# Kernel tuning notes

Measured on AMD Instinct MI355X. Metric: run time of the kernel, lower is better.

The kernel has to match this reference:

```python
import jax, jax.numpy as jnp
import numpy as np

IOU_TH = 0.5      # iou_threshold
SCORE_TH = 0.5    # confidence_threshold (passed as score_threshold to tf NMS)
MAX_DET = 512     # max_detections


def setup_inputs() -> dict:
    key = jax.random.key(0)
    k1, k2, k3 = jax.random.split(key, 3)
    B, N, C = 8, 2048, 80
    # tf.image.non_max_suppression interprets box columns as corners
    # (y1, x1, y2, x2); generate valid corner boxes in [0, 1].
    mins = jax.random.uniform(k1, (B, N, 2), dtype=jnp.float32)
    sizes = jax.random.uniform(k2, (B, N, 2), dtype=jnp.float32) * 0.2 + 0.01
    box_prediction = jnp.concatenate([mins, mins + sizes], axis=-1)  # [B,N,4]
    class_prediction = jax.random.normal(k3, (B, N, C), dtype=jnp.float32) * 2.0
    return {"box_prediction": box_prediction, "class_prediction": class_prediction}


def _nms_single(boxes, cls_pred, conf):
    """Greedy NMS for one image. boxes [N,4], cls_pred [N,C], conf [N].
    Matches tf.image.non_max_suppression semantics (corner-coordinate IoU,
    score threshold, greedy suppression in descending score order),
    then gathers boxes/cls/conf at the kept indices, padded to MAX_DET."""
    N = boxes.shape[0]
    order = jnp.argsort(-conf)                 # descending scores
    b = boxes[order]                            # [N,4]
    c = cls_pred[order]                         # [N,C]
    s = conf[order]                             # [N]

    bb = jax.lax.stop_gradient(b)               # IoU/indices are non-diff
    y1, x1, y2, x2 = bb[:, 0], bb[:, 1], bb[:, 2], bb[:, 3]
    area = (y2 - y1) * (x2 - x1)                # [N]
    ih = jnp.clip(jnp.minimum(y2[:, None], y2[None, :]) -
                  jnp.maximum(y1[:, None], y1[None, :]), 0.0)
    iw = jnp.clip(jnp.minimum(x2[:, None], x2[None, :]) -
                  jnp.maximum(x1[:, None], x1[None, :]), 0.0)
    inter = ih * iw                             # [N,N]
    union = area[:, None] + area[None, :] - inter
    iou = inter / jnp.maximum(union, 1e-9)      # [N,N]

    valid = s > SCORE_TH                        # score_threshold filter
    idxs = jnp.arange(N)

    def step(keep, xs):
        row, i = xs
        # if box i survives, suppress all later boxes overlapping > IOU_TH
        sup = (row > IOU_TH) & (idxs > i) & keep[i]
        return keep & ~sup, None

    keep, _ = jax.lax.scan(step, valid, (iou, idxs))

    # select kept boxes (already sorted by score) padded to MAX_DET
    masked = jnp.where(keep, s, -1.0)
    top_s, top_idx = jax.lax.top_k(jax.lax.stop_gradient(masked), MAX_DET)
    vm = top_s > SCORE_TH                       # validity of each output slot
    out_box = b[top_idx] * vm[:, None].astype(b.dtype)
    out_cls = c[top_idx] * vm[:, None].astype(c.dtype)
    out_conf = jnp.where(vm, s[top_idx], 0.0)
    return out_box, out_cls, out_conf


def reference(box_prediction, class_prediction):
    # from_logits=True branch of the layer
    class_confidence = jnp.max(jax.nn.sigmoid(class_prediction), axis=-1)  # [B,N]
    cls_prob = jax.nn.softmax(class_prediction, axis=-1)                   # [B,N,C]
    nms_box, nms_cls, nms_conf = jax.vmap(_nms_single)(
        box_prediction, cls_prob, class_confidence)
    return nms_box, nms_cls, nms_conf
```

## Files before the change

kernel.cpp:

```cpp
#include <hip/hip_runtime.h>
#include <stdint.h>

#define BB 8
#define NN 2048
#define NC 80
#define MAXDET 512
#define WPR 32


#define ORD_HALF 0xBF000000u

__global__ void k_conf(const float* __restrict__ cls, uint64_t* __restrict__ keys) {
    int gid = blockIdx.x * blockDim.x + threadIdx.x;
    const float4* p = (const float4*)(cls + (size_t)gid * NC);
    float m = -3.0e38f;
#pragma unroll
    for (int i = 0; i < NC / 4; ++i) {
        float4 v = p[i];
        m = fmaxf(m, fmaxf(fmaxf(v.x, v.y), fmaxf(v.z, v.w)));
    }
    float e  = expf(-m);
    float cf = 1.0f / (1.0f + e);
    uint32_t u = __float_as_uint(cf);
    u = (u & 0x80000000u) ? ~u : (u | 0x80000000u);
    int n = gid & (NN - 1);
    keys[gid] = ((uint64_t)u << 32) | (uint32_t)(NN - 1 - n);
}

#define RCHUNK 128
__global__ __launch_bounds__(512) void k_rank(const uint64_t* __restrict__ keys_in,
                                              uint64_t* __restrict__ keys_out,
                                              const float* __restrict__ boxes,
                                              float* __restrict__ sboxes) {
    __shared__ uint64_t sk[NN];
    __shared__ uint16_t part[4][RCHUNK];
    int b = blockIdx.y, t = threadIdx.x;
    const uint64_t* kin = keys_in + (size_t)b * NN;
#pragma unroll
    for (int j = 0; j < NN / 512; ++j)
        sk[t + j * 512] = kin[t + j * 512];
    __syncthreads();
    int sub = t >> 7;
    int el  = t & (RCHUNK - 1);
    int e   = blockIdx.x * RCHUNK + el;
    uint64_t mykey = sk[e];
    int base = sub * (NN / 4);
    int r = 0;
    for (int mm = 0; mm < NN / 4; ++mm)
        r += (sk[base + mm] > mykey) ? 1 : 0;
    part[sub][el] = (uint16_t)r;
    __syncthreads();
    if (t < RCHUNK) {
        int rank = part[0][t] + part[1][t] + part[2][t] + part[3][t];
        keys_out[(size_t)b * NN + rank] = mykey;
        int orig = (NN - 1) - (int)(mykey & 0xFFFFFFFFull);
        ((float4*)sboxes)[(size_t)b * NN + rank] =
            ((const float4*)boxes)[(size_t)b * NN + orig];
    }
}

__global__ void k_sup(const float* __restrict__ sboxes, uint64_t* __restrict__ sup) {
#pragma clang fp contract(off)
    __shared__ float cy1[256], cx1[256], cy2[256], cx2[256], car[256];
    __shared__ float ry1[64], rx1[64], ry2[64], rx2[64], rar[64];
    int rt = blockIdx.x, ct = blockIdx.y, b = blockIdx.z;
    int t = threadIdx.x;
    int col0 = ct << 8, row0 = rt << 6;
    {
        float4 bx = ((const float4*)sboxes)[(size_t)b * NN + col0 + t];
        cy1[t] = bx.x; cx1[t] = bx.y; cy2[t] = bx.z; cx2[t] = bx.w;
        car[t] = (bx.z - bx.x) * (bx.w - bx.y);
        if (t < 64) {
            float4 rb = ((const float4*)sboxes)[(size_t)b * NN + row0 + t];
            ry1[t] = rb.x; rx1[t] = rb.y; ry2[t] = rb.z; rx2[t] = rb.w;
            rar[t] = (rb.z - rb.x) * (rb.w - rb.y);
        }
    }
    __syncthreads();
    int lr = t & 63, lg = t >> 6;
    int r = row0 + lr;
    int gw = (ct << 2) + lg;
    int cbase = gw << 6;
    uint64_t w = 0;
    if (cbase + 63 > r) {
        float y1 = ry1[lr], x1 = rx1[lr], y2 = ry2[lr], x2 = rx2[lr], ar = rar[lr];
        int lcb = lg << 6;
        for (int c = 0; c < 64; ++c) {
            int lc = lcb + c;
            float ih = fmaxf(fminf(y2, cy2[lc]) - fmaxf(y1, cy1[lc]), 0.0f);
            float iw = fmaxf(fminf(x2, cx2[lc]) - fmaxf(x1, cx1[lc]), 0.0f);
            float inter = ih * iw;
            float uni = (ar + car[lc]) - inter;
            float iou = inter / fmaxf(uni, 1e-9f);
            if ((iou > 0.5f) & ((cbase + c) > r)) w |= (1ull << c);
        }
    }
    sup[((size_t)b * NN + r) * WPR + gw] = w;
}

#define NMS_THREADS 256
__global__ __launch_bounds__(NMS_THREADS) void k_nms(const uint64_t* __restrict__ keys,
                                                     const float* __restrict__ sboxes,
                                                     const uint64_t* __restrict__ sup,
                                                     int* __restrict__ kidx,
                                                     int* __restrict__ kcount,
                                                     float* __restrict__ out_box,
                                                     float* __restrict__ out_conf) {
    __shared__ uint64_t buf[2][64 * WPR];
    __shared__ uint8_t  val[NN];
    __shared__ uint64_t kmaskS[WPR];
    __shared__ int pfx[WPR];
    __shared__ int s_kc;
    __shared__ int s_done;
    int b = blockIdx.x, t = threadIdx.x;
    const uint64_t* supb = sup + (size_t)b * NN * WPR;
    const uint64_t* keyb = keys + (size_t)b * NN;

    for (int i = t; i < NN; i += NMS_THREADS)
        val[i] = (uint8_t)((uint32_t)(keyb[i] >> 32) > ORD_HALF);
    if (t < WPR) kmaskS[t] = 0;
    if (t == 0) s_done = 0;
    for (int w = t; w < 64 * WPR; w += NMS_THREADS)
        buf[0][w] = supb[w];
    __syncthreads();

    int wave = t >> 6;
    uint64_t kb = 0;
    int cnt = 0;
    if (t < 32) {
        uint64_t vm = 0;
#pragma unroll
        for (int c = 0; c < 64; ++c)
            vm |= ((uint64_t)val[(t << 6) | c]) << c;
        kb = ~vm;
    }

    for (int g = 0; g < WPR; ++g) {
        if (wave > 0) {
            if (g + 1 < WPR) {
                const uint64_t* src = supb + (size_t)(g + 1) * 64 * WPR;
                uint64_t* dst = buf[(g + 1) & 1];
                for (int w = t - 64; w < 64 * WPR; w += (NMS_THREADS - 64))
                    dst[w] = src[w];
            }
        } else if (t < 32) {
            const int l = t;
            const uint64_t* bufc = buf[g & 1];
            uint64_t rw = __shfl(kb, g);
            uint64_t gm = 0;
#pragma unroll
            for (int c = 0; c < 64; ++c) {
                uint64_t rowg = bufc[c * WPR + g];
                uint64_t rowl = bufc[c * WPR + l];
                bool kept = (((rw >> c) & 1ull) == 0);
                if (kept) {
                    rw |= rowg;
                    kb |= rowl;
                    gm |= (1ull << c);
                }
            }
            if (l == g) kmaskS[g] = gm;
            cnt += __popcll(gm);
            if (cnt >= MAXDET) s_done = 1;
        }
        __syncthreads();
        if (s_done) break;
    }

    if (t == 0) {
        int s = 0;
        for (int w2 = 0; w2 < WPR; ++w2) { pfx[w2] = s; s += __popcll(kmaskS[w2]); }
        s_kc = (s < MAXDET) ? s : MAXDET;
        kcount[b] = s_kc;
    }
    __syncthreads();
    for (int i = t; i < NN; i += NMS_THREADS) {
        uint64_t m = kmaskS[i >> 6];
        if ((m >> (i & 63)) & 1ull) {
            int rank = pfx[i >> 6] + __popcll(m & ((1ull << (i & 63)) - 1ull));
            if (rank < MAXDET) {
                ((float4*)out_box)[(size_t)b * MAXDET + rank] =
                    ((const float4*)sboxes)[(size_t)b * NN + i];
                uint64_t kk = keyb[i];
                uint32_t u = (uint32_t)(kk >> 32);
                float cf = (u & 0x80000000u) ? __uint_as_float(u ^ 0x80000000u)
                                             : __uint_as_float(~u);
                out_conf[(size_t)b * MAXDET + rank] = cf;
                kidx[b * MAXDET + rank] = (NN - 1) - (int)(kk & 0xFFFFFFFFull);
            }
        }
    }
    for (int k = s_kc + t; k < MAXDET; k += NMS_THREADS) {
        ((float4*)out_box)[(size_t)b * MAXDET + k] = make_float4(0.f, 0.f, 0.f, 0.f);
        out_conf[(size_t)b * MAXDET + k] = 0.0f;
    }
}

__global__ void k_softmax(const float* __restrict__ cls, const int* __restrict__ kidx,
                          const int* __restrict__ kcount, float* __restrict__ out_cls) {
    int k = blockIdx.x, b = blockIdx.y, lane = threadIdx.x;
    float* dst = out_cls + ((size_t)b * MAXDET + k) * NC;
    if (k >= kcount[b]) {
        dst[lane] = 0.0f;
        if (lane < NC - 64) dst[64 + lane] = 0.0f;
        return;
    }
    int n = kidx[b * MAXDET + k];
    const float* src = cls + ((size_t)b * NN + n) * NC;
    float x0 = src[lane];
    float x1 = (lane < NC - 64) ? src[64 + lane] : -3.0e38f;
    float m = fmaxf(x0, x1);
    for (int o = 32; o > 0; o >>= 1) m = fmaxf(m, __shfl_xor(m, o));
    float e0 = expf(x0 - m);
    float e1 = (lane < NC - 64) ? expf(x1 - m) : 0.0f;
    float s = e0 + e1;
    for (int o = 32; o > 0; o >>= 1) s += __shfl_xor(s, o);
    dst[lane] = e0 / s;
    if (lane < NC - 64) dst[64 + lane] = e1 / s;
}

extern "C" void kernel_launch(void* const* d_in, const int* in_sizes, int n_in,
                              void* d_out, int out_size, void* d_ws, size_t ws_size,
                              hipStream_t stream) {
    const float* boxes = (const float*)d_in[0];
    const float* cls   = (const float*)d_in[1];
    float* out      = (float*)d_out;
    float* out_box  = out;
    float* out_cls  = out + BB * MAXDET * 4;
    float* out_conf = out + BB * MAXDET * (4 + NC);

    char* ws = (char*)d_ws;
    uint64_t* keysA  = (uint64_t*)(ws + 0);
    uint64_t* keysB  = (uint64_t*)(ws + 131072);
    float*    sboxes = (float*)(ws + 262144);
    int*      kidx   = (int*)(ws + 524288);
    int*      kcount = (int*)(ws + 540672);
    uint64_t* sup    = (uint64_t*)(ws + 544768);

    k_conf<<<(BB * NN) / 256, 256, 0, stream>>>(cls, keysA);
    k_rank<<<dim3(NN / RCHUNK, BB), 512, 0, stream>>>(keysA, keysB, boxes, sboxes);
    k_sup<<<dim3(NN / 64, NN / 256, BB), 256, 0, stream>>>(sboxes, sup);
    k_nms<<<BB, NMS_THREADS, 0, stream>>>(keysB, sboxes, sup, kidx, kcount, out_box, out_conf);
    k_softmax<<<dim3(MAXDET, BB), 64, 0, stream>>>(cls, kidx, kcount, out_cls);
}
```

Before: 90.77 us.

## Replace sequential greedy NMS scan with parallel fixed-point iteration over keep mask

```diff
diff --git a/kernel.cpp b/kernel.cpp
--- a/kernel.cpp
+++ b/kernel.cpp
@@ -10,8 +10,9 @@
 
 #define ORD_HALF 0xBF000000u
 
-__global__ void k_conf(const float* __restrict__ cls, uint64_t* __restrict__ keys) {
-    int gid = blockIdx.x * blockDim.x + threadIdx.x;
+__global__ __launch_bounds__(64) void k_conf(const float* __restrict__ cls,
+                                             uint64_t* __restrict__ keys) {
+    int gid = blockIdx.x * 64 + threadIdx.x;
     const float4* p = (const float4*)(cls + (size_t)gid * NC);
     float m = -3.0e38f;
 #pragma unroll
@@ -98,7 +99,7 @@
     sup[((size_t)b * NN + r) * WPR + gw] = w;
 }
 
-#define NMS_THREADS 256
+#define NMS_THREADS 512
 __global__ __launch_bounds__(NMS_THREADS) void k_nms(const uint64_t* __restrict__ keys,
                                                      const float* __restrict__ sboxes,
                                                      const uint64_t* __restrict__ sup,
@@ -106,76 +107,62 @@
                                                      int* __restrict__ kcount,
                                                      float* __restrict__ out_box,
                                                      float* __restrict__ out_conf) {
-    __shared__ uint64_t buf[2][64 * WPR];
-    __shared__ uint8_t  val[NN];
-    __shared__ uint64_t kmaskS[WPR];
+    __shared__ uint64_t keepW[WPR], validW[WPR];
+    __shared__ uint64_t part[16][WPR + 1];
     __shared__ int pfx[WPR];
     __shared__ int s_kc;
-    __shared__ int s_done;
+    __shared__ int s_changed;
     int b = blockIdx.x, t = threadIdx.x;
     const uint64_t* supb = sup + (size_t)b * NN * WPR;
     const uint64_t* keyb = keys + (size_t)b * NN;
 
-    for (int i = t; i < NN; i += NMS_THREADS)
-        val[i] = (uint8_t)((uint32_t)(keyb[i] >> 32) > ORD_HALF);
-    if (t < WPR) kmaskS[t] = 0;
-    if (t == 0) s_done = 0;
-    for (int w = t; w < 64 * WPR; w += NMS_THREADS)
-        buf[0][w] = supb[w];
-    __syncthreads();
-
-    int wave = t >> 6;
-    uint64_t kb = 0;
-    int cnt = 0;
-    if (t < 32) {
-        uint64_t vm = 0;
-#pragma unroll
-        for (int c = 0; c < 64; ++c)
-            vm |= ((uint64_t)val[(t << 6) | c]) << c;
-        kb = ~vm;
-    }
-
-    for (int g = 0; g < WPR; ++g) {
-        if (wave > 0) {
-            if (g + 1 < WPR) {
-                const uint64_t* src = supb + (size_t)(g + 1) * 64 * WPR;
-                uint64_t* dst = buf[(g + 1) & 1];
-                for (int w = t - 64; w < 64 * WPR; w += (NMS_THREADS - 64))
-                    dst[w] = src[w];
-            }
-        } else if (t < 32) {
-            const int l = t;
-            const uint64_t* bufc = buf[g & 1];
-            uint64_t rw = __shfl(kb, g);
-            uint64_t gm = 0;
-#pragma unroll
-            for (int c = 0; c < 64; ++c) {
-                uint64_t rowg = bufc[c * WPR + g];
-                uint64_t rowl = bufc[c * WPR + l];
-                bool kept = (((rw >> c) & 1ull) == 0);
-                if (kept) {
-                    rw |= rowg;
-                    kb |= rowl;
-                    gm |= (1ull << c);
-                }
-            }
-            if (l == g) kmaskS[g] = gm;
-            cnt += __popcll(gm);
-            if (cnt >= MAXDET) s_done = 1;
-        }
+    {
+        int wv = t >> 6, lane = t & 63;
+#pragma unroll
+        for (int i = 0; i < 4; ++i) {
+            int wi = (wv << 2) + i;
+            uint32_t hi = (uint32_t)(keyb[(wi << 6) + lane] >> 32);
+            uint64_t bal = __ballot(hi > ORD_HALF);
+            if (lane == 0) { validW[wi] = bal; keepW[wi] = bal; }
+        }
+    }
+    __syncthreads();
+
+    int chunk = t >> 5, w = t & 31;
+    const uint64_t* supc = supb + ((size_t)(chunk << 7)) * WPR + w;
+    for (int iter = 0; iter < NN; ++iter) {
+        uint64_t k0 = keepW[chunk << 1];
+        uint64_t k1 = keepW[(chunk << 1) + 1];
+        uint64_t acc = 0;
+#pragma unroll 4
+        for (int j2 = 0; j2 < 64; ++j2)
+            if ((k0 >> j2) & 1ull) acc |= supc[(size_t)j2 * WPR];
+#pragma unroll 4
+        for (int j2 = 0; j2 < 64; ++j2)
+            if ((k1 >> j2) & 1ull) acc |= supc[(size_t)(j2 + 64) * WPR];
+        part[chunk][w] = acc;
+        if (t == 0) s_changed = 0;
         __syncthreads();
-        if (s_done) break;
+        if (t < WPR) {
+            uint64_t rm = 0;
+#pragma unroll
+            for (int c = 0; c < 16; ++c) rm |= part[c][t];
+            uint64_t nk = validW[t] & ~rm;
+            if (nk != keepW[t]) { keepW[t] = nk; s_changed = 1; }
+        }
+        __syncthreads();
+        if (!s_changed) break;
     }
 
     if (t == 0) {
         int s = 0;
-        for (int w2 = 0; w2 < WPR; ++w2) { pfx[w2] = s; s += __popcll(kmaskS[w2]); }
+        for (int w2 = 0; w2 < WPR; ++w2) { pfx[w2] = s; s += __popcll(keepW[w2]); }
         s_kc = (s < MAXDET) ? s : MAXDET;
         kcount[b] = s_kc;
     }
     __syncthreads();
     for (int i = t; i < NN; i += NMS_THREADS) {
-        uint64_t m = kmaskS[i >> 6];
+        uint64_t m = keepW[i >> 6];
         if ((m >> (i & 63)) & 1ull) {
             int rank = pfx[i >> 6] + __popcll(m & ((1ull << (i & 63)) - 1ull));
             if (rank < MAXDET) {
@@ -237,7 +224,7 @@
     int*      kcount = (int*)(ws + 540672);
     uint64_t* sup    = (uint64_t*)(ws + 544768);
 
-    k_conf<<<(BB * NN) / 256, 256, 0, stream>>>(cls, keysA);
+    k_conf<<<(BB * NN) / 64, 64, 0, stream>>>(cls, keysA);
     k_rank<<<dim3(NN / RCHUNK, BB), 512, 0, stream>>>(keysA, keysB, boxes, sboxes);
     k_sup<<<dim3(NN / 64, NN / 256, BB), 256, 0, stream>>>(sboxes, sup);
     k_nms<<<BB, NMS_THREADS, 0, stream>>>(keysB, sboxes, sup, kidx, kcount, out_box, out_conf);
```

New measurement: 171.3 us. 1.89x slower.
